# Kernel tuning notes

Measured on AMD Instinct MI355X. Metric: run time of the kernel, lower is better.

The kernel has to match this reference:

```python
import jax, jax.numpy as jnp
import numpy as np
from jax import lax

H = 20  # hidden size hardcoded in BayesianNN


def setup_inputs() -> dict:
    key = jax.random.key(0)
    ks = jax.random.split(key, 8)
    B, T, D = 256, 2048, 32
    x = jax.random.normal(ks[0], (B, T, D), dtype=jnp.float32)
    w_ih_mu = jax.random.normal(ks[1], (D, 4 * H), dtype=jnp.float32) * 0.1
    w_ih_rho = jnp.full((D, 4 * H), -3.0, dtype=jnp.float32)
    w_ih_eps = jax.random.normal(ks[2], (D, 4 * H), dtype=jnp.float32)
    w_hh_mu = jax.random.normal(ks[3], (H, 4 * H), dtype=jnp.float32) * 0.1
    w_hh_rho = jnp.full((H, 4 * H), -3.0, dtype=jnp.float32)
    w_hh_eps = jax.random.normal(ks[4], (H, 4 * H), dtype=jnp.float32)
    b_mu = jnp.zeros((4 * H,), dtype=jnp.float32)
    b_rho = jnp.full((4 * H,), -3.0, dtype=jnp.float32)
    b_eps = jax.random.normal(ks[5], (4 * H,), dtype=jnp.float32)
    w_lin = jax.random.normal(ks[6], (H, 1), dtype=jnp.float32) * 0.1
    b_lin = jnp.zeros((1,), dtype=jnp.float32)
    return {"x": x, "w_ih_mu": w_ih_mu, "w_ih_rho": w_ih_rho, "w_ih_eps": w_ih_eps,
            "w_hh_mu": w_hh_mu, "w_hh_rho": w_hh_rho, "w_hh_eps": w_hh_eps,
            "b_mu": b_mu, "b_rho": b_rho, "b_eps": b_eps,
            "w_lin": w_lin, "b_lin": b_lin}


def _sample(mu, rho, eps):
    # blitz TrainableRandomDistribution: sigma = log1p(exp(rho))
    return mu + jnp.log1p(jnp.exp(rho)) * eps


def reference(x, w_ih_mu, w_ih_rho, w_ih_eps, w_hh_mu, w_hh_rho, w_hh_eps,
              b_mu, b_rho, b_eps, w_lin, b_lin):
    w_ih = _sample(w_ih_mu, w_ih_rho, w_ih_eps)   # (D, 4H)
    w_hh = _sample(w_hh_mu, w_hh_rho, w_hh_eps)   # (H, 4H)
    bias = _sample(b_mu, b_rho, b_eps)            # (4H,)
    B = x.shape[0]
    # precompute the input-to-gate projection for all timesteps at once
    xg = jnp.einsum('btd,dg->btg', x, w_ih) + bias  # (B, T, 4H)

    def step(carry, xg_t):
        h, c = carry
        gates = xg_t + h @ w_hh                   # (B, 4H)
        i, f, g, o = jnp.split(gates, 4, axis=-1)
        i = jax.nn.sigmoid(i)
        f = jax.nn.sigmoid(f)
        g = jnp.tanh(g)
        o = jax.nn.sigmoid(o)
        c = f * c + i * g
        h = o * jnp.tanh(c)
        return (h, c), h

    h0 = jnp.zeros((B, H), dtype=x.dtype)
    c0 = jnp.zeros((B, H), dtype=x.dtype)
    (_, _), hs = lax.scan(step, (h0, c0), jnp.swapaxes(xg, 0, 1))  # hs: (T, B, H)
    h_seq = jnp.swapaxes(hs, 0, 1)                # (B, T, H)
    out = h_seq @ w_lin + b_lin                   # (B, T, 1)
    return out
```

## Files before the change

### kernel.cpp

```cpp
#include <hip/hip_runtime.h>
#include <hip/hip_bf16.h>
#include <math.h>

#define TSEQ 2048
#define DIN  32
#define HID  20
#define G4   80
#define TILE 16
#define NT   (TSEQ / TILE)
#define HSTR 68
#define L2E  1.44269504088896340736f

typedef float v2f __attribute__((ext_vector_type(2)));
typedef unsigned int uint2v __attribute__((ext_vector_type(2)));
typedef _Float16 h2v __attribute__((ext_vector_type(2)));

#if __has_builtin(__builtin_amdgcn_exp2f)
#define EXP2(x) __builtin_amdgcn_exp2f(x)
#else
#define EXP2(x) __expf((x) * 0.69314718055994531f)
#endif

#if __has_builtin(__builtin_amdgcn_fdot2) && \
    (__has_builtin(__builtin_amdgcn_mov_dpp) || __has_builtin(__builtin_amdgcn_update_dpp)) && \
    __has_builtin(__builtin_amdgcn_perm)
#define USE_FDOT2 1
#else
#define USE_FDOT2 0
#endif

__device__ __forceinline__ float rl(float v, int l) {
    return __int_as_float(__builtin_amdgcn_readlane(__float_as_int(v), l));
}

__device__ __forceinline__ float sig2(float xs) {
    return __builtin_amdgcn_rcpf(1.0f + EXP2(-xs));
}

__device__ __forceinline__ float xhalf(float v) {
#if __has_builtin(__builtin_amdgcn_permlane32_swap)
    uint2v r = __builtin_amdgcn_permlane32_swap(__float_as_uint(v),
                                                __float_as_uint(v),
                                                false, false);
    return (__uint_as_float(r.x) + __uint_as_float(r.y)) - v;
#else
    return __shfl_xor(v, 32);
#endif
}

__device__ __forceinline__ float samp(const float* mu, const float* rho,
                                      const float* eps, int i) {
    return mu[i] + log1pf(__expf(rho[i])) * eps[i];
}

__device__ __forceinline__ int dpp_odd_to_even(int v) {
#if __has_builtin(__builtin_amdgcn_mov_dpp)
    return __builtin_amdgcn_mov_dpp(v, 0xF5, 0xf, 0xf, false);
#else
    return __builtin_amdgcn_update_dpp(0, v, 0xF5, 0xf, 0xf, false);
#endif
}

__global__ __launch_bounds__(128, 1) void blstm_fused(
    const float* __restrict__ x,
    const float* __restrict__ wih_mu, const float* __restrict__ wih_rho, const float* __restrict__ wih_eps,
    const float* __restrict__ whh_mu, const float* __restrict__ whh_rho, const float* __restrict__ whh_eps,
    const float* __restrict__ bmu,    const float* __restrict__ brho,    const float* __restrict__ beps,
    const float* __restrict__ wlin,   const float* __restrict__ blin,
    float* __restrict__ out)
{
    __shared__ __align__(16) float lds_xg[2][TILE * G4];
    __shared__ __align__(16) float lds_x[TILE * DIN];
    __shared__ __align__(16) float hist[64 * HSTR];

    const int tid  = threadIdx.x;
    const int lane = tid & 63;
    const int b    = blockIdx.x;
    const float* xrow = x + (size_t)b * TSEQ * DIN;
    float* outp = out + (size_t)b * TSEQ;

    if (tid < 64) {
        const int p  = lane >> 5;
        const int k  = lane & 31;
        const int ke = (k < HID) ? k : (HID - 1);
        const int g1 = p * 40 + ke;
        const int g2 = g1 + HID;
        const float sc1 = (p ? 2.0f : 1.0f) * L2E;
        const float sc2 = L2E;
        const float aAct2 = p ? (4.0f * L2E) : 1.0f;
        const float cAct2 = p ? (-2.0f * L2E) : 0.0f;

#if USE_FDOT2
        h2v w1h[HID / 2], w2h[HID / 2];
#pragma unroll
        for (int m = 0; m < HID / 2; ++m) {
            const int je = 2 * m, jo = 2 * m + 1;
            w1h[m] = (h2v){ (_Float16)(samp(whh_mu, whh_rho, whh_eps, je * G4 + g1) * sc1),
                            (_Float16)(samp(whh_mu, whh_rho, whh_eps, jo * G4 + g1) * sc1) };
            w2h[m] = (h2v){ (_Float16)(samp(whh_mu, whh_rho, whh_eps, je * G4 + g2) * sc2),
                            (_Float16)(samp(whh_mu, whh_rho, whh_eps, jo * G4 + g2) * sc2) };
        }
#else
        v2f w12e[HID / 2], w12o[HID / 2];
#pragma unroll
        for (int jj = 0; jj < HID / 2; ++jj) {
            const int je = 2 * jj, jo = 2 * jj + 1;
            w12e[jj] = (v2f){ samp(whh_mu, whh_rho, whh_eps, je * G4 + g1) * sc1,
                              samp(whh_mu, whh_rho, whh_eps, je * G4 + g2) * sc2 };
            w12o[jj] = (v2f){ samp(whh_mu, whh_rho, whh_eps, jo * G4 + g1) * sc1,
                              samp(whh_mu, whh_rho, whh_eps, jo * G4 + g2) * sc2 };
        }
#endif
        const int coff = p * 40 + ke * 2;

        float h = 0.0f, c = 0.0f;
        for (int kt = 0; kt < NT; ++kt) {
            __syncthreads();
            const float* xg = lds_xg[kt & 1];
            v2f xgr[TILE];
#pragma unroll
            for (int r = 0; r < TILE; ++r)
                xgr[r] = *(const v2f*)&xg[r * G4 + coff];

#pragma unroll
            for (int ti = 0; ti < TILE; ++ti) {
                float d1, d2;
#if USE_FDOT2
                const _Float16 hf = (_Float16)h;
                const unsigned cv = (unsigned)__builtin_bit_cast(unsigned short, hf);
                const int      sh = dpp_odd_to_even((int)cv);
                const unsigned pk = __builtin_amdgcn_perm((unsigned)sh, cv, 0x05040100u);

                int hp[HID / 2];
#pragma unroll
                for (int m = 0; m < HID / 2; ++m)
                    hp[m] = __builtin_amdgcn_readlane((int)pk, 2 * m);

                float d1a = xgr[ti].x, d2a = xgr[ti].y;
                float d1b = 0.0f, d2b = 0.0f;
#pragma unroll
                for (int m = 0; m < 5; ++m) {
                    const h2v hv = __builtin_bit_cast(h2v, hp[m]);
                    d1a = __builtin_amdgcn_fdot2(hv, w1h[m], d1a, false);
                    d2a = __builtin_amdgcn_fdot2(hv, w2h[m], d2a, false);
                }
#pragma unroll
                for (int m = 5; m < HID / 2; ++m) {
                    const h2v hv = __builtin_bit_cast(h2v, hp[m]);
                    d1b = __builtin_amdgcn_fdot2(hv, w1h[m], d1b, false);
                    d2b = __builtin_amdgcn_fdot2(hv, w2h[m], d2b, false);
                }
                d1 = d1a + d1b;
                d2 = d2a + d2b;
#else
                float hj[HID];
#pragma unroll
                for (int j = 0; j < HID; ++j) hj[j] = rl(h, j);

                v2f d12a = xgr[ti];
                v2f d12b = (v2f){0.0f, 0.0f};
#pragma unroll
                for (int jj = 0; jj < HID / 2; ++jj) {
                    d12a = __builtin_elementwise_fma(
                        (v2f){hj[2 * jj], hj[2 * jj]}, w12e[jj], d12a);
                    d12b = __builtin_elementwise_fma(
                        (v2f){hj[2 * jj + 1], hj[2 * jj + 1]}, w12o[jj], d12b);
                }
                const v2f d12 = d12a + d12b;
                d1 = d12.x;
                d2 = d12.y;
#endif

                const float s1   = sig2(d1);
                const float act1 = fmaf(s1, aAct2, cAct2);
                const float act2 = sig2(d2);

                const float og1 = xhalf(act1);
                const float og2 = xhalf(act2);

                c = fmaf(act2, c, act1 * og1);
                const float tc = fmaf(2.0f, sig2(c), -1.0f);
                h = og2 * tc;

                const int t = kt * TILE + ti;
                hist[(t & 63) * HSTR + lane] = h;
            }
        }
        __syncthreads();
    } else {
        const int cA = lane;
        const int cB = 64 + (lane & 15);
        const float scA = ((cA >= 40 && cA < 60) ? 2.0f : 1.0f) * L2E;
        const float scB = L2E;

        float wA[DIN], wB[DIN];
#pragma unroll
        for (int d = 0; d < DIN; ++d) {
            wA[d] = samp(wih_mu, wih_rho, wih_eps, d * G4 + cA) * scA;
            wB[d] = samp(wih_mu, wih_rho, wih_eps, d * G4 + cB) * scB;
        }
        const float biasA = samp(bmu, brho, beps, cA) * scA;
        const float biasB = samp(bmu, brho, beps, cB) * scB;

        const int posA = ((cA >= 40) ? 40 : 0) + (cA % 20) * 2 + ((cA / 20) & 1);
        const int posB = ((cB >= 40) ? 40 : 0) + (cB % 20) * 2 + ((cB / 20) & 1);
        const int qs   = (lane >> 4) * 4;

        float wl[HID];
#pragma unroll
        for (int j = 0; j < HID; ++j) wl[j] = wlin[j];
        const float bl = blin[0];

        auto produce = [&](int kt) {
            const float* xu = xrow + kt * TILE * DIN;
            float* xgb = lds_xg[kt & 1];
            {
                const float4* src = (const float4*)xu;
                float4 v0 = src[lane * 2 + 0];
                float4 v1 = src[lane * 2 + 1];
                ((float4*)lds_x)[lane * 2 + 0] = v0;
                ((float4*)lds_x)[lane * 2 + 1] = v1;
            }
#pragma unroll
            for (int s = 0; s < TILE; ++s) {
                float a0 = 0.0f, a1 = 0.0f;
#pragma unroll
                for (int d = 0; d < 16; ++d) {
                    a0 = fmaf(xu[s * DIN + d],      wA[d],      a0);
                    a1 = fmaf(xu[s * DIN + d + 16], wA[d + 16], a1);
                }
                xgb[s * G4 + posA] = biasA + a0 + a1;
            }
#pragma unroll
            for (int jj = 0; jj < 4; ++jj) {
                const int s = qs + jj;
                const float4* xr = (const float4*)&lds_x[s * DIN];
                float a0 = 0.0f, a1 = 0.0f;
#pragma unroll
                for (int q = 0; q < 4; ++q) {
                    const float4 u0 = xr[q], u1 = xr[q + 4];
                    a0 = fmaf(u0.x, wB[q * 4 + 0],      a0);
                    a0 = fmaf(u0.y, wB[q * 4 + 1],      a0);
                    a0 = fmaf(u0.z, wB[q * 4 + 2],      a0);
                    a0 = fmaf(u0.w, wB[q * 4 + 3],      a0);
                    a1 = fmaf(u1.x, wB[16 + q * 4 + 0], a1);
                    a1 = fmaf(u1.y, wB[16 + q * 4 + 1], a1);
                    a1 = fmaf(u1.z, wB[16 + q * 4 + 2], a1);
                    a1 = fmaf(u1.w, wB[16 + q * 4 + 3], a1);
                }
                xgb[s * G4 + posB] = biasB + a0 + a1;
            }
        };

        auto flush = [&](int ft) {
            if (lane < TILE) {
                const int t = ft * TILE + lane;
                const float4* hr = (const float4*)&hist[(t & 63) * HSTR];
                const float4 r0 = hr[0], r1 = hr[1], r2 = hr[2], r3 = hr[3], r4 = hr[4];
                float acc = bl;
                acc = fmaf(r0.x, wl[0],  acc); acc = fmaf(r0.y, wl[1],  acc);
                acc = fmaf(r0.z, wl[2],  acc); acc = fmaf(r0.w, wl[3],  acc);
                acc = fmaf(r1.x, wl[4],  acc); acc = fmaf(r1.y, wl[5],  acc);
                acc = fmaf(r1.z, wl[6],  acc); acc = fmaf(r1.w, wl[7],  acc);
                acc = fmaf(r2.x, wl[8],  acc); acc = fmaf(r2.y, wl[9],  acc);
                acc = fmaf(r2.z, wl[10], acc); acc = fmaf(r2.w, wl[11], acc);
                acc = fmaf(r3.x, wl[12], acc); acc = fmaf(r3.y, wl[13], acc);
                acc = fmaf(r3.z, wl[14], acc); acc = fmaf(r3.w, wl[15], acc);
                acc = fmaf(r4.x, wl[16], acc); acc = fmaf(r4.y, wl[17], acc);
                acc = fmaf(r4.z, wl[18], acc); acc = fmaf(r4.w, wl[19], acc);
                outp[t] = acc;
            }
        };

        produce(0);
        for (int kt = 0; kt < NT; ++kt) {
            __syncthreads();
            if (kt + 1 < NT) produce(kt + 1);
            if (kt >= 1)     flush(kt - 1);
        }
        __syncthreads();
        flush(NT - 1);
    }
}

extern "C" void kernel_launch(void* const* d_in, const int* in_sizes, int n_in,
                              void* d_out, int out_size, void* d_ws, size_t ws_size,
                              hipStream_t stream) {
    const float* x       = (const float*)d_in[0];
    const float* wih_mu  = (const float*)d_in[1];
    const float* wih_rho = (const float*)d_in[2];
    const float* wih_eps = (const float*)d_in[3];
    const float* whh_mu  = (const float*)d_in[4];
    const float* whh_rho = (const float*)d_in[5];
    const float* whh_eps = (const float*)d_in[6];
    const float* bmu     = (const float*)d_in[7];
    const float* brho    = (const float*)d_in[8];
    const float* beps    = (const float*)d_in[9];
    const float* wlin    = (const float*)d_in[10];
    const float* blin    = (const float*)d_in[11];
    float* out = (float*)d_out;

    const int B = in_sizes[0] / (TSEQ * DIN);

    blstm_fused<<<B, 128, 0, stream>>>(x, wih_mu, wih_rho, wih_eps,
                                       whh_mu, whh_rho, whh_eps,
                                       bmu, brho, beps, wlin, blin, out);
}
```

Baseline: 393.3 us.

## Interleave two batch sequences per block to hide recurrence latency

Each block now processes two independent batch rows, interleaving their LSTM recurrences step by step so the dependent readlane/fdot2/exp chains of one sequence can fill the latency bubbles of the other. The grid shrinks from B to B/2 blocks. LDS buffers double and the producer wave does twice the projection work per tile. With 256 rows and many CUs this halves the parallelism, so the trade depends on whether per-step latency or the number of concurrent sequences is the limit.

```diff
diff --git a/kernel.cpp b/kernel.cpp
--- a/kernel.cpp
+++ b/kernel.cpp
@@ -61,23 +61,26 @@
 #endif
 }
 
-__global__ __launch_bounds__(128, 1) void blstm_fused(
+__global__ __launch_bounds__(128, 1) void blstm_pair(
     const float* __restrict__ x,
     const float* __restrict__ wih_mu, const float* __restrict__ wih_rho, const float* __restrict__ wih_eps,
     const float* __restrict__ whh_mu, const float* __restrict__ whh_rho, const float* __restrict__ whh_eps,
     const float* __restrict__ bmu,    const float* __restrict__ brho,    const float* __restrict__ beps,
     const float* __restrict__ wlin,   const float* __restrict__ blin,
-    float* __restrict__ out)
+    float* __restrict__ out, int B)
 {
-    __shared__ __align__(16) float lds_xg[2][TILE * G4];
-    __shared__ __align__(16) float lds_x[TILE * DIN];
-    __shared__ __align__(16) float hist[64 * HSTR];
+    __shared__ __align__(16) float lds_xg[2][2][TILE * G4];
+    __shared__ __align__(16) float lds_x[2][TILE * DIN];
+    __shared__ __align__(16) float hist[2][64 * HSTR];
 
     const int tid  = threadIdx.x;
     const int lane = tid & 63;
-    const int b    = blockIdx.x;
-    const float* xrow = x + (size_t)b * TSEQ * DIN;
-    float* outp = out + (size_t)b * TSEQ;
+    const int bA   = blockIdx.x * 2;
+    const int bB   = (bA + 1 < B) ? (bA + 1) : bA;
+    const float* xrowA = x + (size_t)bA * TSEQ * DIN;
+    const float* xrowB = x + (size_t)bB * TSEQ * DIN;
+    float* outA = out + (size_t)bA * TSEQ;
+    float* outB = out + (size_t)bB * TSEQ;
 
     if (tid < 64) {
         const int p  = lane >> 5;
@@ -113,97 +116,123 @@
 #endif
         const int coff = p * 40 + ke * 2;
 
-        float h = 0.0f, c = 0.0f;
+        float hA = 0.0f, cA = 0.0f, hB = 0.0f, cB = 0.0f;
         for (int kt = 0; kt < NT; ++kt) {
             __syncthreads();
-            const float* xg = lds_xg[kt & 1];
-            v2f xgr[TILE];
-#pragma unroll
-            for (int r = 0; r < TILE; ++r)
-                xgr[r] = *(const v2f*)&xg[r * G4 + coff];
+            const float* xgpA = lds_xg[0][kt & 1];
+            const float* xgpB = lds_xg[1][kt & 1];
+            v2f xgrA[TILE], xgrB[TILE];
+#pragma unroll
+            for (int r = 0; r < TILE; ++r) {
+                xgrA[r] = *(const v2f*)&xgpA[r * G4 + coff];
+                xgrB[r] = *(const v2f*)&xgpB[r * G4 + coff];
+            }
 
 #pragma unroll
             for (int ti = 0; ti < TILE; ++ti) {
-                float d1, d2;
+                const int t = kt * TILE + ti;
+                float d1A, d2A, d1B, d2B;
 #if USE_FDOT2
-                const _Float16 hf = (_Float16)h;
-                const unsigned cv = (unsigned)__builtin_bit_cast(unsigned short, hf);
-                const int      sh = dpp_odd_to_even((int)cv);
-                const unsigned pk = __builtin_amdgcn_perm((unsigned)sh, cv, 0x05040100u);
-
-                int hp[HID / 2];
-#pragma unroll
-                for (int m = 0; m < HID / 2; ++m)
-                    hp[m] = __builtin_amdgcn_readlane((int)pk, 2 * m);
-
-                float d1a = xgr[ti].x, d2a = xgr[ti].y;
-                float d1b = 0.0f, d2b = 0.0f;
+                const _Float16 hfA = (_Float16)hA;
+                const _Float16 hfB = (_Float16)hB;
+                const unsigned cvA = (unsigned)__builtin_bit_cast(unsigned short, hfA);
+                const unsigned cvB = (unsigned)__builtin_bit_cast(unsigned short, hfB);
+                const int      shA = dpp_odd_to_even((int)cvA);
+                const int      shB = dpp_odd_to_even((int)cvB);
+                const unsigned pkA = __builtin_amdgcn_perm((unsigned)shA, cvA, 0x05040100u);
+                const unsigned pkB = __builtin_amdgcn_perm((unsigned)shB, cvB, 0x05040100u);
+
+                int hpA[HID / 2], hpB[HID / 2];
+#pragma unroll
+                for (int m = 0; m < HID / 2; ++m) {
+                    hpA[m] = __builtin_amdgcn_readlane((int)pkA, 2 * m);
+                    hpB[m] = __builtin_amdgcn_readlane((int)pkB, 2 * m);
+                }
+
+                float d1aA = xgrA[ti].x, d2aA = xgrA[ti].y;
+                float d1aB = xgrB[ti].x, d2aB = xgrB[ti].y;
+                float d1bA = 0.0f, d2bA = 0.0f, d1bB = 0.0f, d2bB = 0.0f;
 #pragma unroll
                 for (int m = 0; m < 5; ++m) {
-                    const h2v hv = __builtin_bit_cast(h2v, hp[m]);
-                    d1a = __builtin_amdgcn_fdot2(hv, w1h[m], d1a, false);
-                    d2a = __builtin_amdgcn_fdot2(hv, w2h[m], d2a, false);
+                    const h2v hvA = __builtin_bit_cast(h2v, hpA[m]);
+                    const h2v hvB = __builtin_bit_cast(h2v, hpB[m]);
+                    d1aA = __builtin_amdgcn_fdot2(hvA, w1h[m], d1aA, false);
+                    d1aB = __builtin_amdgcn_fdot2(hvB, w1h[m], d1aB, false);
+                    d2aA = __builtin_amdgcn_fdot2(hvA, w2h[m], d2aA, false);
+                    d2aB = __builtin_amdgcn_fdot2(hvB, w2h[m], d2aB, false);
                 }
 #pragma unroll
                 for (int m = 5; m < HID / 2; ++m) {
-                    const h2v hv = __builtin_bit_cast(h2v, hp[m]);
-                    d1b = __builtin_amdgcn_fdot2(hv, w1h[m], d1b, false);
-                    d2b = __builtin_amdgcn_fdot2(hv, w2h[m], d2b, false);
-                }
-                d1 = d1a + d1b;
-                d2 = d2a + d2b;
-#else
-                float hj[HID];
-#pragma unroll
-                for (int j = 0; j < HID; ++j) hj[j] = rl(h, j);
-
-                v2f d12a = xgr[ti];
-                v2f d12b = (v2f){0.0f, 0.0f};
+                    const h2v hvA = __builtin_bit_cast(h2v, hpA[m]);
+                    const h2v hvB = __builtin_bit_cast(h2v, hpB[m]);
+                    d1bA = __builtin_amdgcn_fdot2(hvA, w1h[m], d1bA, false);
+                    d1bB = __builtin_amdgcn_fdot2(hvB, w1h[m], d1bB, false);
+                    d2bA = __builtin_amdgcn_fdot2(hvA, w2h[m], d2bA, false);
+                    d2bB = __builtin_amdgcn_fdot2(hvB, w2h[m], d2bB, false);
+                }
+                d1A = d1aA + d1bA;  d2A = d2aA + d2bA;
+                d1B = d1aB + d1bB;  d2B = d2aB + d2bB;
+#else
+                float hjA[HID], hjB[HID];
+#pragma unroll
+                for (int j = 0; j < HID; ++j) {
+                    hjA[j] = rl(hA, j);
+                    hjB[j] = rl(hB, j);
+                }
+                v2f dA1 = xgrA[ti], dA2 = (v2f){0.0f, 0.0f};
+                v2f dB1 = xgrB[ti], dB2 = (v2f){0.0f, 0.0f};
 #pragma unroll
                 for (int jj = 0; jj < HID / 2; ++jj) {
-                    d12a = __builtin_elementwise_fma(
-                        (v2f){hj[2 * jj], hj[2 * jj]}, w12e[jj], d12a);
-                    d12b = __builtin_elementwise_fma(
-                        (v2f){hj[2 * jj + 1], hj[2 * jj + 1]}, w12o[jj], d12b);
-                }
-                const v2f d12 = d12a + d12b;
-                d1 = d12.x;
-                d2 = d12.y;
-#endif
-
-                const float s1   = sig2(d1);
-                const float act1 = fmaf(s1, aAct2, cAct2);
-                const float act2 = sig2(d2);
-
-                const float og1 = xhalf(act1);
-                const float og2 = xhalf(act2);
-
-                c = fmaf(act2, c, act1 * og1);
-                const float tc = fmaf(2.0f, sig2(c), -1.0f);
-                h = og2 * tc;
-
-                const int t = kt * TILE + ti;
-                hist[(t & 63) * HSTR + lane] = h;
+                    dA1 = __builtin_elementwise_fma((v2f){hjA[2*jj], hjA[2*jj]}, w12e[jj], dA1);
+                    dB1 = __builtin_elementwise_fma((v2f){hjB[2*jj], hjB[2*jj]}, w12e[jj], dB1);
+                    dA2 = __builtin_elementwise_fma((v2f){hjA[2*jj+1], hjA[2*jj+1]}, w12o[jj], dA2);
+                    dB2 = __builtin_elementwise_fma((v2f){hjB[2*jj+1], hjB[2*jj+1]}, w12o[jj], dB2);
+                }
+                const v2f dSA = dA1 + dA2, dSB = dB1 + dB2;
+                d1A = dSA.x; d2A = dSA.y; d1B = dSB.x; d2B = dSB.y;
+#endif
+
+                const float s1A   = sig2(d1A);
+                const float s1B   = sig2(d1B);
+                const float act1A = fmaf(s1A, aAct2, cAct2);
+                const float act1B = fmaf(s1B, aAct2, cAct2);
+                const float act2A = sig2(d2A);
+                const float act2B = sig2(d2B);
+
+                const float og1A = xhalf(act1A);
+                const float og1B = xhalf(act1B);
+                const float og2A = xhalf(act2A);
+                const float og2B = xhalf(act2B);
+
+                cA = fmaf(act2A, cA, act1A * og1A);
+                cB = fmaf(act2B, cB, act1B * og1B);
+                const float tcA = fmaf(2.0f, sig2(cA), -1.0f);
+                const float tcB = fmaf(2.0f, sig2(cB), -1.0f);
+                hA = og2A * tcA;
+                hB = og2B * tcB;
+
+                hist[0][(t & 63) * HSTR + lane] = hA;
+                hist[1][(t & 63) * HSTR + lane] = hB;
             }
         }
         __syncthreads();
     } else {
-        const int cA = lane;
-        const int cB = 64 + (lane & 15);
-        const float scA = ((cA >= 40 && cA < 60) ? 2.0f : 1.0f) * L2E;
+        const int cAc = lane;
+        const int cBc = 64 + (lane & 15);
+        const float scA = ((cAc >= 40 && cAc < 60) ? 2.0f : 1.0f) * L2E;
         const float scB = L2E;
 
         float wA[DIN], wB[DIN];
 #pragma unroll
         for (int d = 0; d < DIN; ++d) {
-            wA[d] = samp(wih_mu, wih_rho, wih_eps, d * G4 + cA) * scA;
-            wB[d] = samp(wih_mu, wih_rho, wih_eps, d * G4 + cB) * scB;
-        }
-        const float biasA = samp(bmu, brho, beps, cA) * scA;
-        const float biasB = samp(bmu, brho, beps, cB) * scB;
-
-        const int posA = ((cA >= 40) ? 40 : 0) + (cA % 20) * 2 + ((cA / 20) & 1);
-        const int posB = ((cB >= 40) ? 40 : 0) + (cB % 20) * 2 + ((cB / 20) & 1);
+            wA[d] = samp(wih_mu, wih_rho, wih_eps, d * G4 + cAc) * scA;
+            wB[d] = samp(wih_mu, wih_rho, wih_eps, d * G4 + cBc) * scB;
+        }
+        const float biasA = samp(bmu, brho, beps, cAc) * scA;
+        const float biasB = samp(bmu, brho, beps, cBc) * scB;
+
+        const int posA = ((cAc >= 40) ? 40 : 0) + (cAc % 20) * 2 + ((cAc / 20) & 1);
+        const int posB = 40 + (cBc % 20) * 2 + 1;
         const int qs   = (lane >> 4) * 4;
 
         float wl[HID];
@@ -211,15 +240,16 @@
         for (int j = 0; j < HID; ++j) wl[j] = wlin[j];
         const float bl = blin[0];
 
-        auto produce = [&](int kt) {
-            const float* xu = xrow + kt * TILE * DIN;
-            float* xgb = lds_xg[kt & 1];
+        auto produce = [&](int sq, int kt) {
+            const float* xu = (sq ? xrowB : xrowA) + kt * TILE * DIN;
+            float* xgb = lds_xg[sq][kt & 1];
+            float* lx  = lds_x[sq];
             {
                 const float4* src = (const float4*)xu;
                 float4 v0 = src[lane * 2 + 0];
                 float4 v1 = src[lane * 2 + 1];
-                ((float4*)lds_x)[lane * 2 + 0] = v0;
-                ((float4*)lds_x)[lane * 2 + 1] = v1;
+                ((float4*)lx)[lane * 2 + 0] = v0;
+                ((float4*)lx)[lane * 2 + 1] = v1;
             }
 #pragma unroll
             for (int s = 0; s < TILE; ++s) {
@@ -234,7 +264,7 @@
 #pragma unroll
             for (int jj = 0; jj < 4; ++jj) {
                 const int s = qs + jj;
-                const float4* xr = (const float4*)&lds_x[s * DIN];
+                const float4* xr = (const float4*)&lx[s * DIN];
                 float a0 = 0.0f, a1 = 0.0f;
 #pragma unroll
                 for (int q = 0; q < 4; ++q) {
@@ -252,10 +282,10 @@
             }
         };
 
-        auto flush = [&](int ft) {
+        auto flush = [&](int sq, int ft) {
             if (lane < TILE) {
                 const int t = ft * TILE + lane;
-                const float4* hr = (const float4*)&hist[(t & 63) * HSTR];
+                const float4* hr = (const float4*)&hist[sq][(t & 63) * HSTR];
                 const float4 r0 = hr[0], r1 = hr[1], r2 = hr[2], r3 = hr[3], r4 = hr[4];
                 float acc = bl;
                 acc = fmaf(r0.x, wl[0],  acc); acc = fmaf(r0.y, wl[1],  acc);
@@ -268,18 +298,26 @@
                 acc = fmaf(r3.z, wl[14], acc); acc = fmaf(r3.w, wl[15], acc);
                 acc = fmaf(r4.x, wl[16], acc); acc = fmaf(r4.y, wl[17], acc);
                 acc = fmaf(r4.z, wl[18], acc); acc = fmaf(r4.w, wl[19], acc);
-                outp[t] = acc;
+                (sq ? outB : outA)[t] = acc;
             }
         };
 
-        produce(0);
+        produce(0, 0);
+        produce(1, 0);
         for (int kt = 0; kt < NT; ++kt) {
             __syncthreads();
-            if (kt + 1 < NT) produce(kt + 1);
-            if (kt >= 1)     flush(kt - 1);
+            if (kt + 1 < NT) {
+                produce(0, kt + 1);
+                produce(1, kt + 1);
+            }
+            if (kt >= 1) {
+                flush(0, kt - 1);
+                flush(1, kt - 1);
+            }
         }
         __syncthreads();
-        flush(NT - 1);
+        flush(0, NT - 1);
+        flush(1, NT - 1);
     }
 }
 
@@ -301,8 +339,9 @@
     float* out = (float*)d_out;
 
     const int B = in_sizes[0] / (TSEQ * DIN);
-
-    blstm_fused<<<B, 128, 0, stream>>>(x, wih_mu, wih_rho, wih_eps,
-                                       whh_mu, whh_rho, whh_eps,
-                                       bmu, brho, beps, wlin, blin, out);
-}
+    const int pairs = (B + 1) / 2;
+
+    blstm_pair<<<pairs, 128, 0, stream>>>(x, wih_mu, wih_rho, wih_eps,
+                                          whh_mu, whh_rho, whh_eps,
+                                          bmu, brho, beps, wlin, blin, out, B);
+}
```

Measured after the change: 824.9 us. 110% more time.
